# Kernel optimization log

Measured on AMD Instinct MI355X. Metric: run time of the kernel, lower is better.

The kernel has to match this reference:

```python
import jax, jax.numpy as jnp
import numpy as np

B, N, L, D, DP, H = 1, 128, 256, 256, 128, 8
DH = D // H
LN_EPS = 1e-5


def setup_inputs() -> dict:
    key = jax.random.key(0)
    ks = jax.random.split(key, 8)
    w = lambda k, shape: jax.random.normal(k, shape, jnp.float32) * 0.02
    return {
        "msa": jax.random.normal(ks[0], (B, N, L, D), jnp.float32),
        "pair_bias": jax.random.normal(ks[1], (B, L, L, DP), jnp.float32),
        "msa_mask": jnp.ones((B, N, L), jnp.int32),
        "ln_g": jnp.ones((D,), jnp.float32),
        "ln_b": jnp.zeros((D,), jnp.float32),
        "Wq": w(ks[2], (D, D)), "bq": jnp.zeros((D,), jnp.float32),
        "Wk": w(ks[3], (D, D)), "bk": jnp.zeros((D,), jnp.float32),
        "Wv": w(ks[4], (D, D)), "bv": jnp.zeros((D,), jnp.float32),
        "Wb": w(ks[5], (DP, H)), "bb": jnp.zeros((H,), jnp.float32),
        "Wo": w(ks[6], (D, D)), "bo": jnp.zeros((D,), jnp.float32),
        # gate initialized as in the torch module: zero weight, ones bias
        "Wg": jnp.zeros((D, D), jnp.float32), "bg": jnp.ones((D,), jnp.float32),
    }


def reference(msa, pair_bias, msa_mask, ln_g, ln_b, Wq, bq, Wk, bk, Wv, bv,
              Wb, bb, Wo, bo, Wg, bg):
    b, n, l, d = msa.shape
    h = bb.shape[0]
    dh = d // h
    # LayerNorm over d_msa
    mu = msa.mean(-1, keepdims=True)
    var = msa.var(-1, keepdims=True)
    xn = (msa - mu) * jax.lax.rsqrt(var + LN_EPS) * ln_g + ln_b
    # projections -> [b, n, l, h, dh]
    q = (xn @ Wq + bq).reshape(b, n, l, h, dh)
    k = (xn @ Wk + bk).reshape(b, n, l, h, dh)
    v = (xn @ Wv + bv).reshape(b, n, l, h, dh)
    scores = jnp.einsum('bnihd,bnjhd->bnhij', q, k) / jnp.sqrt(jnp.float32(dh))
    # pair bias: [b, l, l, h] -> [b, 1, h, l, l], broadcast over N_seq
    bias = (pair_bias @ Wb + bb).transpose(0, 3, 1, 2)[:, None]
    scores = scores + bias
    # mask over key axis
    mask = msa_mask[:, :, None, None, :].astype(bool)
    scores = jnp.where(mask, scores, jnp.float32(-1e9))
    attn = jax.nn.softmax(scores, axis=-1)  # dropout is identity at eval
    out = jnp.einsum('bnhij,bnjhd->bnihd', attn, v).reshape(b, n, l, d)
    out = out @ Wo + bo
    gate = jax.nn.sigmoid(xn @ Wg + bg)
    return out * gate
```

## Files before the change

### kernel.cpp

```cpp
#include <hip/hip_runtime.h>
#include <hip/hip_bf16.h>

typedef __attribute__((ext_vector_type(4))) float f32x4;
typedef __attribute__((ext_vector_type(16))) float f32x16;
typedef __attribute__((ext_vector_type(8))) __bf16 bf16x8;
typedef __attribute__((ext_vector_type(4))) __bf16 bf16x4;
typedef __attribute__((ext_vector_type(2))) __bf16 bf16x2;
typedef __attribute__((ext_vector_type(4))) unsigned u32x4;
typedef __attribute__((ext_vector_type(2))) unsigned u32x2;

#define VTS 264
#define KLS 40
#define L2E 1.4426950408889634f

#define GLOAD_LDS16(g, l) __builtin_amdgcn_global_load_lds( \
    (const __attribute__((address_space(1))) void*)(g),     \
    (__attribute__((address_space(3))) void*)(l), 16, 0, 0)

#if __has_builtin(__builtin_amdgcn_permlane32_swap)
#define SWP(a, b) { u32x2 _r = __builtin_amdgcn_permlane32_swap((a), (b), false, false); \
                    (a) = _r[0]; (b) = _r[1]; }
#else
#define SWP(a, b) { unsigned _sa = __shfl_xor((a), 32), _sb = __shfl_xor((b), 32); \
                    unsigned _na = hi ? _sb : (a); (b) = hi ? (b) : _sa; (a) = _na; }
#endif
#define SUM32(ts, lrun) { (lrun) += (ts) + __shfl_xor((ts), 32); }

__global__ __launch_bounds__(256) void setup_kernel(
    const float* __restrict__ msa, const float* __restrict__ g,
    const float* __restrict__ b, __bf16* __restrict__ xn,
    const float* __restrict__ pair, const float* __restrict__ Wb,
    const float* __restrict__ bb, float* __restrict__ biasf,
    const float* __restrict__ Wq, const float* __restrict__ Wk,
    const float* __restrict__ Wv, const float* __restrict__ Wg,
    const float* __restrict__ Wo, __bf16* __restrict__ Wt)
{
  __shared__ float wbs[1024];
  const int bid = blockIdx.x;
  const int t = threadIdx.x;
  if (bid < 8192) {
    const int row = bid * 4 + (t >> 6);
    const int lane = t & 63;
    f32x4 x = *(const f32x4*)(msa + (size_t)row * 256 + lane * 4);
    float s = x[0] + x[1] + x[2] + x[3];
    float s2 = x[0]*x[0] + x[1]*x[1] + x[2]*x[2] + x[3]*x[3];
#pragma unroll
    for (int d = 32; d >= 1; d >>= 1) {
      s  += __shfl_xor(s, d);
      s2 += __shfl_xor(s2, d);
    }
    const float mu  = s * (1.f / 256.f);
    const float inv = rsqrtf(s2 * (1.f / 256.f) - mu * mu + 1e-5f);
    const f32x4 gv = *(const f32x4*)(g + lane * 4);
    const f32x4 bv = *(const f32x4*)(b + lane * 4);
    bf16x4 o;
#pragma unroll
    for (int j = 0; j < 4; ++j) o[j] = (__bf16)((x[j] - mu) * inv * gv[j] + bv[j]);
    *(bf16x4*)(xn + (size_t)row * 256 + lane * 4) = o;
  } else if (bid < 8448) {
#pragma unroll
    for (int r2 = 0; r2 < 4; ++r2) wbs[t + 256 * r2] = Wb[t + 256 * r2];
    __syncthreads();
    const int i = bid - 8192, j = t;
    const float* src = pair + ((size_t)i * 256 + j) * 128;
    float acc[8];
#pragma unroll
    for (int hh = 0; hh < 8; ++hh) acc[hh] = bb[hh];
    for (int p = 0; p < 128; p += 4) {
      const f32x4 pv = *(const f32x4*)(src + p);
#pragma unroll
      for (int q2 = 0; q2 < 4; ++q2)
#pragma unroll
        for (int hh = 0; hh < 8; ++hh) acc[hh] += pv[q2] * wbs[(p + q2) * 8 + hh];
    }
#pragma unroll
    for (int hh = 0; hh < 8; ++hh)
      biasf[((size_t)hh * 256 + i) * 256 + j] = acc[hh] * L2E;
  } else {
    const int idx = bid - 8448;
    const int w = idx >> 8, n2 = idx & 255, k = t;
    const float* W = (w == 0) ? Wq : (w == 1) ? Wk : (w == 2) ? Wv : (w == 3) ? Wg : Wo;
    Wt[((size_t)w * 256 + n2) * 256 + k] = (__bf16)W[(size_t)k * 256 + n2];
  }
}

__global__ __launch_bounds__(512, 4) void qkvg_gemm(
    const __bf16* __restrict__ xn, const __bf16* __restrict__ Wt,
    const float* __restrict__ bq, const float* __restrict__ bk,
    const float* __restrict__ bv, const float* __restrict__ bg,
    __bf16* __restrict__ qb, __bf16* __restrict__ kb,
    __bf16* __restrict__ vb, __bf16* __restrict__ gateb)
{
  __shared__ alignas(16) __bf16 Al[256 * 64];
  __shared__ alignas(16) __bf16 Bl[128 * 64];
  const int t = threadIdx.x;
  const int wave = t >> 6, lane = t & 63;
  const int l15 = lane & 15, l16 = lane >> 4;
  const int bid = blockIdx.x;
  const int xcd = bid & 7, idx = bid >> 3;
  const int m0 = (xcd * 16 + (idx & 15)) * 256;
  const int bn = idx >> 4;
  const int w = bn >> 1;
  const int nloc0 = (bn & 1) * 128;
  const __bf16* Wtw = Wt + (size_t)w * 65536;
  const int wm = (wave >> 1) * 64, wn = (wave & 1) * 64;

  const int srow = (lane >> 3);
  const int chunk = ((lane & 7) ^ srow) * 8;

  f32x4 acc[4][4];
#pragma unroll
  for (int i = 0; i < 4; ++i)
#pragma unroll
    for (int j = 0; j < 4; ++j) acc[i][j] = (f32x4){0.f, 0.f, 0.f, 0.f};

  for (int kt = 0; kt < 4; ++kt) {
    const int k0 = kt * 64;
#pragma unroll
    for (int i = 0; i < 4; ++i) {
      const int row = (wave * 4 + i) * 8 + srow;
      GLOAD_LDS16(xn + (size_t)(m0 + row) * 256 + k0 + chunk, &Al[(wave * 4 + i) * 512]);
    }
#pragma unroll
    for (int i = 0; i < 2; ++i) {
      const int row = (wave * 2 + i) * 8 + srow;
      GLOAD_LDS16(Wtw + (size_t)(nloc0 + row) * 256 + k0 + chunk, &Bl[(wave * 2 + i) * 512]);
    }
    __syncthreads();
#pragma unroll
    for (int kk = 0; kk < 2; ++kk) {
      bf16x8 a[4], bfr[4];
#pragma unroll
      for (int mi = 0; mi < 4; ++mi) {
        const int row = wm + mi * 16 + l15;
        a[mi] = *(const bf16x8*)&Al[row * 64 + ((kk * 32 + l16 * 8) ^ ((row & 7) << 3))];
      }
#pragma unroll
      for (int ni = 0; ni < 4; ++ni) {
        const int row = wn + ni * 16 + l15;
        bfr[ni] = *(const bf16x8*)&Bl[row * 64 + ((kk * 32 + l16 * 8) ^ ((row & 7) << 3))];
      }
#pragma unroll
      for (int mi = 0; mi < 4; ++mi)
#pragma unroll
        for (int ni = 0; ni < 4; ++ni)
          acc[mi][ni] = __builtin_amdgcn_mfma_f32_16x16x32_bf16(a[mi], bfr[ni], acc[mi][ni], 0, 0, 0);
    }
    __syncthreads();
  }

  const float* bias_arr = (w == 0) ? bq : (w == 1) ? bk : (w == 2) ? bv : bg;
  float bnis[4];
#pragma unroll
  for (int ni = 0; ni < 4; ++ni) bnis[ni] = bias_arr[nloc0 + wn + ni * 16 + l15];
  const float qscale = 0.17677669529663687f * L2E;

#pragma unroll
  for (int mi = 0; mi < 4; ++mi)
#pragma unroll
    for (int ni = 0; ni < 4; ++ni)
#pragma unroll
      for (int r = 0; r < 4; ++r) {
        const int grow = m0 + wm + mi * 16 + l16 * 4 + r;
        const int gcol = nloc0 + wn + ni * 16 + l15;
        const float v = acc[mi][ni][r] + bnis[ni];
        const int n = grow >> 8, i2 = grow & 255, h = gcol >> 5, dh = gcol & 31;
        const size_t hoff = (((size_t)n * 8 + h) * 256 + i2) * 32 + dh;
        if (w == 0)      qb[hoff] = (__bf16)(v * qscale);
        else if (w == 1) kb[hoff] = (__bf16)v;
        else if (w == 2) vb[hoff] = (__bf16)v;
        else gateb[(size_t)grow * 256 + gcol] = (__bf16)(1.f / (1.f + __expf(-v)));
      }
}

__device__ __forceinline__ unsigned pk2(float a, float b) {
  bf16x2 t; t[0] = (__bf16)a; t[1] = (__bf16)b;
  return __builtin_bit_cast(unsigned, t);
}

__global__ __launch_bounds__(512, 4) void attn_kernel(
    const __bf16* __restrict__ qb, const __bf16* __restrict__ kb,
    const __bf16* __restrict__ vb, const float* __restrict__ biasf,
    const int* __restrict__ mask, __bf16* __restrict__ opre)
{
  __shared__ alignas(16) __bf16 Kl[256 * KLS];
  __shared__ alignas(16) __bf16 Vt[32 * VTS];
  __shared__ alignas(16) float Ml[256];
  const int t = threadIdx.x, wave = t >> 6, lane = t & 63;
  const int l31 = lane & 31, hi = lane >> 5;
  const int nh = blockIdx.x;
  const int n = nh >> 3, h = nh & 7;
  const __bf16* qbh = qb + (size_t)nh * 8192;

  if (t < 256) {
    const bf16x8* ks = (const bf16x8*)(kb + (size_t)nh * 8192 + t * 32);
    bf16x8 kr[4];
#pragma unroll
    for (int j = 0; j < 4; ++j) kr[j] = ks[j];
#pragma unroll
    for (int j = 0; j < 4; ++j) *(bf16x8*)&Kl[t * KLS + j * 8] = kr[j];
    const bf16x8* vs = (const bf16x8*)(vb + (size_t)nh * 8192 + t * 32);
    bf16x8 vv[4];
#pragma unroll
    for (int j = 0; j < 4; ++j) vv[j] = vs[j];
#pragma unroll
    for (int j = 0; j < 4; ++j)
#pragma unroll
      for (int e = 0; e < 8; ++e) Vt[(j * 8 + e) * VTS + t] = vv[j][e];
    Ml[t] = mask[n * 256 + t] ? 0.f : -1e9f;
  }
  __syncthreads();

  const int q0 = wave * 32;
  const int q = q0 + l31;
  const bf16x8 Qf0 = *(const bf16x8*)(qbh + (size_t)q * 32 + hi * 8);
  const bf16x8 Qf1 = *(const bf16x8*)(qbh + (size_t)q * 32 + 16 + hi * 8);

  const float* bp = biasf + (size_t)h * 65536 + (size_t)q * 256;

  f32x4 bc[4];
#pragma unroll
  for (int g = 0; g < 4; ++g) {
    const f32x4 bv = *(const f32x4*)(bp + 8 * g + 4 * hi);
    const f32x4 mk = *(const f32x4*)&Ml[8 * g + 4 * hi];
    bc[g] = bv + mk;
  }

  f32x16 Ot;
#pragma unroll
  for (int r = 0; r < 16; ++r) Ot[r] = 0.f;
  float lrun = 0.f;

#pragma unroll 1
  for (int kt = 0; kt < 8; ++kt) {
    const int k0 = kt * 32;
    const int ktn = (kt + 1) & 7;
    const bf16x8 Kf0 = *(const bf16x8*)&Kl[(k0 + l31) * KLS + hi * 8];
    const bf16x8 Kf1 = *(const bf16x8*)&Kl[(k0 + l31) * KLS + 16 + hi * 8];
    const bf16x8 Vf0 = *(const bf16x8*)&Vt[l31 * VTS + k0 + hi * 8];
    const bf16x8 Vf1 = *(const bf16x8*)&Vt[l31 * VTS + k0 + 16 + hi * 8];
    f32x16 st;
#pragma unroll
    for (int g = 0; g < 4; ++g)
#pragma unroll
      for (int e = 0; e < 4; ++e) st[4 * g + e] = bc[g][e];
    st = __builtin_amdgcn_mfma_f32_32x32x16_bf16(Kf0, Qf0, st, 0, 0, 0);
    st = __builtin_amdgcn_mfma_f32_32x32x16_bf16(Kf1, Qf1, st, 0, 0, 0);
#pragma unroll
    for (int g = 0; g < 4; ++g) {
      const f32x4 bv = *(const f32x4*)(bp + ktn * 32 + 8 * g + 4 * hi);
      const f32x4 mk = *(const f32x4*)&Ml[ktn * 32 + 8 * g + 4 * hi];
      bc[g] = bv + mk;
    }
#pragma unroll
    for (int r = 0; r < 16; ++r) st[r] = exp2f(st[r]);
    float ts = st[0];
#pragma unroll
    for (int r = 1; r < 16; ++r) ts += st[r];
    SUM32(ts, lrun);
    unsigned c0 = pk2(st[0],  st[1]),  c1 = pk2(st[2],  st[3]);
    unsigned c2 = pk2(st[4],  st[5]),  c3 = pk2(st[6],  st[7]);
    unsigned c4 = pk2(st[8],  st[9]),  c5 = pk2(st[10], st[11]);
    unsigned c6 = pk2(st[12], st[13]), c7 = pk2(st[14], st[15]);
    SWP(c0, c2); SWP(c1, c3); SWP(c4, c6); SWP(c5, c7);
    u32x4 w0 = {c0, c1, c2, c3}, w1 = {c4, c5, c6, c7};
    const bf16x8 pf0 = __builtin_bit_cast(bf16x8, w0);
    const bf16x8 pf1 = __builtin_bit_cast(bf16x8, w1);
    Ot = __builtin_amdgcn_mfma_f32_32x32x16_bf16(Vf0, pf0, Ot, 0, 0, 0);
    Ot = __builtin_amdgcn_mfma_f32_32x32x16_bf16(Vf1, pf1, Ot, 0, 0, 0);
  }

  const float invl = 1.f / lrun;
  unsigned P00 = pk2(Ot[0]  * invl, Ot[1]  * invl), P01 = pk2(Ot[2]  * invl, Ot[3]  * invl);
  unsigned P10 = pk2(Ot[4]  * invl, Ot[5]  * invl), P11 = pk2(Ot[6]  * invl, Ot[7]  * invl);
  unsigned P20 = pk2(Ot[8]  * invl, Ot[9]  * invl), P21 = pk2(Ot[10] * invl, Ot[11] * invl);
  unsigned P30 = pk2(Ot[12] * invl, Ot[13] * invl), P31 = pk2(Ot[14] * invl, Ot[15] * invl);
  SWP(P00, P20); SWP(P01, P21); SWP(P10, P30); SWP(P11, P31);
  u32x4 s0 = {P00, P01, P20, P21}, s1 = {P10, P11, P30, P31};
  __bf16* dst = opre + (((size_t)h * 128 + n) * 256 + q) * 32 + hi * 16;
  *(u32x4*)dst = s0;
  *(u32x4*)(dst + 8) = s1;
}

__global__ __launch_bounds__(256) void wo_gemm(
    const __bf16* __restrict__ A, const __bf16* __restrict__ Wtw,
    const float* __restrict__ bo, const __bf16* __restrict__ gateb,
    float* __restrict__ out)
{
  __shared__ alignas(16) __bf16 Al[128 * 64];
  __shared__ alignas(16) __bf16 Bl[128 * 64];
  const int t = threadIdx.x;
  const int wave = t >> 6, lane = t & 63;
  const int l15 = lane & 15, l16 = lane >> 4;
  const int bid = blockIdx.x;
  const int xcd = bid & 7, idx = bid >> 3;
  const int m0 = (xcd * 32 + (idx & 31)) * 128;
  const int nloc0 = (idx >> 5) * 128;
  const int wm = (wave >> 1) * 64, wn = (wave & 1) * 64;

  const int srow = (lane >> 3);
  const int chunk = ((lane & 7) ^ srow) * 8;

  f32x4 acc[4][4];
#pragma unroll
  for (int i = 0; i < 4; ++i)
#pragma unroll
    for (int j = 0; j < 4; ++j) acc[i][j] = (f32x4){0.f, 0.f, 0.f, 0.f};

  for (int kt = 0; kt < 4; ++kt) {
    const int k0 = kt * 64;
#pragma unroll
    for (int i = 0; i < 4; ++i) {
      const int row = wave * 32 + i * 8 + srow;
      const int m = m0 + row;
      const int kg = k0 + chunk;
      GLOAD_LDS16(A + (size_t)(kg >> 5) * 1048576 + (size_t)(m >> 8) * 8192
                    + (m & 255) * 32 + (kg & 31),
                  &Al[(wave * 4 + i) * 512]);
      GLOAD_LDS16(Wtw + (size_t)(nloc0 + row) * 256 + kg, &Bl[(wave * 4 + i) * 512]);
    }
    __syncthreads();
#pragma unroll
    for (int kk = 0; kk < 2; ++kk) {
      bf16x8 a[4], bfr[4];
#pragma unroll
      for (int mi = 0; mi < 4; ++mi) {
        const int row = wm + mi * 16 + l15;
        a[mi] = *(const bf16x8*)&Al[row * 64 + ((kk * 32 + l16 * 8) ^ ((row & 7) << 3))];
      }
#pragma unroll
      for (int ni = 0; ni < 4; ++ni) {
        const int row = wn + ni * 16 + l15;
        bfr[ni] = *(const bf16x8*)&Bl[row * 64 + ((kk * 32 + l16 * 8) ^ ((row & 7) << 3))];
      }
#pragma unroll
      for (int mi = 0; mi < 4; ++mi)
#pragma unroll
        for (int ni = 0; ni < 4; ++ni)
          acc[mi][ni] = __builtin_amdgcn_mfma_f32_16x16x32_bf16(a[mi], bfr[ni], acc[mi][ni], 0, 0, 0);
    }
    __syncthreads();
  }

  float bov[4];
#pragma unroll
  for (int ni = 0; ni < 4; ++ni) bov[ni] = bo[nloc0 + wn + ni * 16 + l15];
#pragma unroll
  for (int mi = 0; mi < 4; ++mi)
#pragma unroll
    for (int ni = 0; ni < 4; ++ni)
#pragma unroll
      for (int r = 0; r < 4; ++r) {
        const int grow = m0 + wm + mi * 16 + l16 * 4 + r;
        const int gcol = nloc0 + wn + ni * 16 + l15;
        const size_t o = (size_t)grow * 256 + gcol;
        out[o] = (acc[mi][ni][r] + bov[ni]) * (float)gateb[o];
      }
}

extern "C" void kernel_launch(void* const* d_in, const int* in_sizes, int n_in,
                              void* d_out, int out_size, void* d_ws, size_t ws_size,
                              hipStream_t stream)
{
  const float* msa  = (const float*)d_in[0];
  const float* pair = (const float*)d_in[1];
  const int*   mask = (const int*)d_in[2];
  const float* ln_g = (const float*)d_in[3];
  const float* ln_b = (const float*)d_in[4];
  const float* Wq = (const float*)d_in[5];  const float* bq = (const float*)d_in[6];
  const float* Wk = (const float*)d_in[7];  const float* bk = (const float*)d_in[8];
  const float* Wv = (const float*)d_in[9];  const float* bv = (const float*)d_in[10];
  const float* Wb = (const float*)d_in[11]; const float* bb = (const float*)d_in[12];
  const float* Wo = (const float*)d_in[13]; const float* bo = (const float*)d_in[14];
  const float* Wg = (const float*)d_in[15]; const float* bg = (const float*)d_in[16];
  float* out = (float*)d_out;

  char* ws = (char*)d_ws;
  __bf16* xn    = (__bf16*)(ws);
  __bf16* qb    = (__bf16*)(ws + 16777216);
  __bf16* kb    = (__bf16*)(ws + 2 * 16777216);
  __bf16* vb    = (__bf16*)(ws + 3 * 16777216);
  __bf16* opre  = (__bf16*)(ws + 4 * 16777216);
  __bf16* Wt    = (__bf16*)(ws + 5 * 16777216);
  __bf16* gateb = (__bf16*)(ws + 5 * 16777216 + 655360);
  float*  biasf = (float*)(ws + 5 * 16777216 + 655360 + 16777216);

  hipLaunchKernelGGL(setup_kernel, dim3(9728), dim3(256), 0, stream,
                     msa, ln_g, ln_b, xn, pair, Wb, bb, biasf, Wq, Wk, Wv, Wg, Wo, Wt);
  hipLaunchKernelGGL(qkvg_gemm,   dim3(1024), dim3(512), 0, stream, xn, Wt, bq, bk, bv, bg, qb, kb, vb, gateb);
  hipLaunchKernelGGL(attn_kernel, dim3(1024), dim3(512), 0, stream, qb, kb, vb, biasf, mask, opre);
  hipLaunchKernelGGL(wo_gemm,     dim3(512),  dim3(256), 0, stream, opre, Wt + 4 * 65536, bo, gateb, out);
}
```

Before: 126.7 us.

## Process two query tiles per wave in attention kernel with 256-thread blocks

Halves the attention block to 4 waves, with each wave handling two 32-row query tiles that share the K/V fragments read from LDS each iteration. All 256 threads now cooperatively stage K, V and mask, so no threads sit idle during the load. The software-prefetched bias registers are dropped; bias is now loaded directly inside the loop. This cuts LDS reads per query and adds independent MFMA chains for ILP, at the cost of more registers per wave and fewer waves per block.

```diff
diff --git a/kernel.cpp b/kernel.cpp
--- a/kernel.cpp
+++ b/kernel.cpp
@@ -178,7 +178,7 @@
   return __builtin_bit_cast(unsigned, t);
 }
 
-__global__ __launch_bounds__(512, 4) void attn_kernel(
+__global__ __launch_bounds__(256, 4) void attn_kernel(
     const __bf16* __restrict__ qb, const __bf16* __restrict__ kb,
     const __bf16* __restrict__ vb, const float* __restrict__ biasf,
     const int* __restrict__ mask, __bf16* __restrict__ opre)
@@ -192,7 +192,7 @@
   const int n = nh >> 3, h = nh & 7;
   const __bf16* qbh = qb + (size_t)nh * 8192;
 
-  if (t < 256) {
+  {
     const bf16x8* ks = (const bf16x8*)(kb + (size_t)nh * 8192 + t * 32);
     bf16x8 kr[4];
 #pragma unroll
@@ -211,75 +211,93 @@
   }
   __syncthreads();
 
-  const int q0 = wave * 32;
-  const int q = q0 + l31;
-  const bf16x8 Qf0 = *(const bf16x8*)(qbh + (size_t)q * 32 + hi * 8);
-  const bf16x8 Qf1 = *(const bf16x8*)(qbh + (size_t)q * 32 + 16 + hi * 8);
-
-  const float* bp = biasf + (size_t)h * 65536 + (size_t)q * 256;
-
-  f32x4 bc[4];
-#pragma unroll
-  for (int g = 0; g < 4; ++g) {
-    const f32x4 bv = *(const f32x4*)(bp + 8 * g + 4 * hi);
-    const f32x4 mk = *(const f32x4*)&Ml[8 * g + 4 * hi];
-    bc[g] = bv + mk;
-  }
-
-  f32x16 Ot;
-#pragma unroll
-  for (int r = 0; r < 16; ++r) Ot[r] = 0.f;
-  float lrun = 0.f;
+  const int qA = wave * 64 + l31;
+  const int qB = qA + 32;
+  const bf16x8 QfA0 = *(const bf16x8*)(qbh + (size_t)qA * 32 + hi * 8);
+  const bf16x8 QfA1 = *(const bf16x8*)(qbh + (size_t)qA * 32 + 16 + hi * 8);
+  const bf16x8 QfB0 = *(const bf16x8*)(qbh + (size_t)qB * 32 + hi * 8);
+  const bf16x8 QfB1 = *(const bf16x8*)(qbh + (size_t)qB * 32 + 16 + hi * 8);
+
+  const float* bpA = biasf + (size_t)h * 65536 + (size_t)qA * 256;
+  const float* bpB = biasf + (size_t)h * 65536 + (size_t)qB * 256;
+
+  f32x16 OtA, OtB;
+#pragma unroll
+  for (int r = 0; r < 16; ++r) { OtA[r] = 0.f; OtB[r] = 0.f; }
+  float lrunA = 0.f, lrunB = 0.f;
 
 #pragma unroll 1
   for (int kt = 0; kt < 8; ++kt) {
     const int k0 = kt * 32;
-    const int ktn = (kt + 1) & 7;
     const bf16x8 Kf0 = *(const bf16x8*)&Kl[(k0 + l31) * KLS + hi * 8];
     const bf16x8 Kf1 = *(const bf16x8*)&Kl[(k0 + l31) * KLS + 16 + hi * 8];
     const bf16x8 Vf0 = *(const bf16x8*)&Vt[l31 * VTS + k0 + hi * 8];
     const bf16x8 Vf1 = *(const bf16x8*)&Vt[l31 * VTS + k0 + 16 + hi * 8];
-    f32x16 st;
-#pragma unroll
-    for (int g = 0; g < 4; ++g)
-#pragma unroll
-      for (int e = 0; e < 4; ++e) st[4 * g + e] = bc[g][e];
-    st = __builtin_amdgcn_mfma_f32_32x32x16_bf16(Kf0, Qf0, st, 0, 0, 0);
-    st = __builtin_amdgcn_mfma_f32_32x32x16_bf16(Kf1, Qf1, st, 0, 0, 0);
+    f32x16 stA, stB;
 #pragma unroll
     for (int g = 0; g < 4; ++g) {
-      const f32x4 bv = *(const f32x4*)(bp + ktn * 32 + 8 * g + 4 * hi);
-      const f32x4 mk = *(const f32x4*)&Ml[ktn * 32 + 8 * g + 4 * hi];
-      bc[g] = bv + mk;
-    }
-#pragma unroll
-    for (int r = 0; r < 16; ++r) st[r] = exp2f(st[r]);
-    float ts = st[0];
-#pragma unroll
-    for (int r = 1; r < 16; ++r) ts += st[r];
-    SUM32(ts, lrun);
-    unsigned c0 = pk2(st[0],  st[1]),  c1 = pk2(st[2],  st[3]);
-    unsigned c2 = pk2(st[4],  st[5]),  c3 = pk2(st[6],  st[7]);
-    unsigned c4 = pk2(st[8],  st[9]),  c5 = pk2(st[10], st[11]);
-    unsigned c6 = pk2(st[12], st[13]), c7 = pk2(st[14], st[15]);
-    SWP(c0, c2); SWP(c1, c3); SWP(c4, c6); SWP(c5, c7);
-    u32x4 w0 = {c0, c1, c2, c3}, w1 = {c4, c5, c6, c7};
-    const bf16x8 pf0 = __builtin_bit_cast(bf16x8, w0);
-    const bf16x8 pf1 = __builtin_bit_cast(bf16x8, w1);
-    Ot = __builtin_amdgcn_mfma_f32_32x32x16_bf16(Vf0, pf0, Ot, 0, 0, 0);
-    Ot = __builtin_amdgcn_mfma_f32_32x32x16_bf16(Vf1, pf1, Ot, 0, 0, 0);
-  }
-
-  const float invl = 1.f / lrun;
-  unsigned P00 = pk2(Ot[0]  * invl, Ot[1]  * invl), P01 = pk2(Ot[2]  * invl, Ot[3]  * invl);
-  unsigned P10 = pk2(Ot[4]  * invl, Ot[5]  * invl), P11 = pk2(Ot[6]  * invl, Ot[7]  * invl);
-  unsigned P20 = pk2(Ot[8]  * invl, Ot[9]  * invl), P21 = pk2(Ot[10] * invl, Ot[11] * invl);
-  unsigned P30 = pk2(Ot[12] * invl, Ot[13] * invl), P31 = pk2(Ot[14] * invl, Ot[15] * invl);
-  SWP(P00, P20); SWP(P01, P21); SWP(P10, P30); SWP(P11, P31);
-  u32x4 s0 = {P00, P01, P20, P21}, s1 = {P10, P11, P30, P31};
-  __bf16* dst = opre + (((size_t)h * 128 + n) * 256 + q) * 32 + hi * 16;
-  *(u32x4*)dst = s0;
-  *(u32x4*)(dst + 8) = s1;
+      const f32x4 mk = *(const f32x4*)&Ml[k0 + 8 * g + 4 * hi];
+      const f32x4 bvA = *(const f32x4*)(bpA + k0 + 8 * g + 4 * hi);
+      const f32x4 bvB = *(const f32x4*)(bpB + k0 + 8 * g + 4 * hi);
+#pragma unroll
+      for (int e = 0; e < 4; ++e) {
+        stA[4 * g + e] = bvA[e] + mk[e];
+        stB[4 * g + e] = bvB[e] + mk[e];
+      }
+    }
+    stA = __builtin_amdgcn_mfma_f32_32x32x16_bf16(Kf0, QfA0, stA, 0, 0, 0);
+    stA = __builtin_amdgcn_mfma_f32_32x32x16_bf16(Kf1, QfA1, stA, 0, 0, 0);
+    stB = __builtin_amdgcn_mfma_f32_32x32x16_bf16(Kf0, QfB0, stB, 0, 0, 0);
+    stB = __builtin_amdgcn_mfma_f32_32x32x16_bf16(Kf1, QfB1, stB, 0, 0, 0);
+    {
+#pragma unroll
+      for (int r = 0; r < 16; ++r) stA[r] = exp2f(stA[r]);
+      float ts = stA[0];
+#pragma unroll
+      for (int r = 1; r < 16; ++r) ts += stA[r];
+      SUM32(ts, lrunA);
+      unsigned c0 = pk2(stA[0],  stA[1]),  c1 = pk2(stA[2],  stA[3]);
+      unsigned c2 = pk2(stA[4],  stA[5]),  c3 = pk2(stA[6],  stA[7]);
+      unsigned c4 = pk2(stA[8],  stA[9]),  c5 = pk2(stA[10], stA[11]);
+      unsigned c6 = pk2(stA[12], stA[13]), c7 = pk2(stA[14], stA[15]);
+      SWP(c0, c2); SWP(c1, c3); SWP(c4, c6); SWP(c5, c7);
+      u32x4 w0 = {c0, c1, c2, c3}, w1 = {c4, c5, c6, c7};
+      OtA = __builtin_amdgcn_mfma_f32_32x32x16_bf16(Vf0, __builtin_bit_cast(bf16x8, w0), OtA, 0, 0, 0);
+      OtA = __builtin_amdgcn_mfma_f32_32x32x16_bf16(Vf1, __builtin_bit_cast(bf16x8, w1), OtA, 0, 0, 0);
+    }
+    {
+#pragma unroll
+      for (int r = 0; r < 16; ++r) stB[r] = exp2f(stB[r]);
+      float ts = stB[0];
+#pragma unroll
+      for (int r = 1; r < 16; ++r) ts += stB[r];
+      SUM32(ts, lrunB);
+      unsigned c0 = pk2(stB[0],  stB[1]),  c1 = pk2(stB[2],  stB[3]);
+      unsigned c2 = pk2(stB[4],  stB[5]),  c3 = pk2(stB[6],  stB[7]);
+      unsigned c4 = pk2(stB[8],  stB[9]),  c5 = pk2(stB[10], stB[11]);
+      unsigned c6 = pk2(stB[12], stB[13]), c7 = pk2(stB[14], stB[15]);
+      SWP(c0, c2); SWP(c1, c3); SWP(c4, c6); SWP(c5, c7);
+      u32x4 w0 = {c0, c1, c2, c3}, w1 = {c4, c5, c6, c7};
+      OtB = __builtin_amdgcn_mfma_f32_32x32x16_bf16(Vf0, __builtin_bit_cast(bf16x8, w0), OtB, 0, 0, 0);
+      OtB = __builtin_amdgcn_mfma_f32_32x32x16_bf16(Vf1, __builtin_bit_cast(bf16x8, w1), OtB, 0, 0, 0);
+    }
+  }
+
+#pragma unroll
+  for (int qt = 0; qt < 2; ++qt) {
+    const f32x16& Ot = qt ? OtB : OtA;
+    const float invl = 1.f / (qt ? lrunB : lrunA);
+    const int q = qt ? qB : qA;
+    unsigned P00 = pk2(Ot[0]  * invl, Ot[1]  * invl), P01 = pk2(Ot[2]  * invl, Ot[3]  * invl);
+    unsigned P10 = pk2(Ot[4]  * invl, Ot[5]  * invl), P11 = pk2(Ot[6]  * invl, Ot[7]  * invl);
+    unsigned P20 = pk2(Ot[8]  * invl, Ot[9]  * invl), P21 = pk2(Ot[10] * invl, Ot[11] * invl);
+    unsigned P30 = pk2(Ot[12] * invl, Ot[13] * invl), P31 = pk2(Ot[14] * invl, Ot[15] * invl);
+    SWP(P00, P20); SWP(P01, P21); SWP(P10, P30); SWP(P11, P31);
+    u32x4 s0 = {P00, P01, P20, P21}, s1 = {P10, P11, P30, P31};
+    __bf16* dst = opre + (((size_t)h * 128 + n) * 256 + q) * 32 + hi * 16;
+    *(u32x4*)dst = s0;
+    *(u32x4*)(dst + 8) = s1;
+  }
 }
 
 __global__ __launch_bounds__(256) void wo_gemm(
@@ -388,6 +406,6 @@
   hipLaunchKernelGGL(setup_kernel, dim3(9728), dim3(256), 0, stream,
                      msa, ln_g, ln_b, xn, pair, Wb, bb, biasf, Wq, Wk, Wv, Wg, Wo, Wt);
   hipLaunchKernelGGL(qkvg_gemm,   dim3(1024), dim3(512), 0, stream, xn, Wt, bq, bk, bv, bg, qb, kb, vb, gateb);
-  hipLaunchKernelGGL(attn_kernel, dim3(1024), dim3(512), 0, stream, qb, kb, vb, biasf, mask, opre);
+  hipLaunchKernelGGL(attn_kernel, dim3(1024), dim3(256), 0, stream, qb, kb, vb, biasf, mask, opre);
   hipLaunchKernelGGL(wo_gemm,     dim3(512),  dim3(256), 0, stream, opre, Wt + 4 * 65536, bo, gateb, out);
 }
```

Result: slower. 130.5 us (+3.0%).
